# Optimization experiments

Hardware: AMD Instinct MI355X
Metric: run time of the kernel (lower is better)

The kernel has to match this reference:

```python
import jax, jax.numpy as jnp
import numpy as np

DIM = 3072
DIM_HEAD = 128
HEADS = 16
KV_DIM = 2048
INNER = DIM_HEAD * HEADS  # 2048


def layernorm(x, g, b, eps=1e-5):
    mu = jnp.mean(x, axis=-1, keepdims=True)
    var = jnp.mean((x - mu) ** 2, axis=-1, keepdims=True)
    return (x - mu) * jax.lax.rsqrt(var + eps) * g + b


def setup_inputs() -> dict:
    key = jax.random.key(0)
    ks = jax.random.split(key, 6)
    b, n1, n2 = 2, 4096, 1024
    x = jax.random.normal(ks[0], (b, n1, KV_DIM), dtype=jnp.float32)
    latents = jax.random.normal(ks[1], (b, n2, DIM), dtype=jnp.float32)
    # Linear weights stored [in, out] (torch stores [out, in]; math is x @ W)
    Wq = jax.random.normal(ks[2], (DIM, INNER), dtype=jnp.float32) * 0.02
    Wkv = jax.random.normal(ks[3], (KV_DIM, 2 * INNER), dtype=jnp.float32) * 0.02
    Wout = jax.random.normal(ks[4], (INNER, DIM), dtype=jnp.float32) * 0.02
    ln1_g = jnp.ones((KV_DIM,), jnp.float32)
    ln1_b = jnp.zeros((KV_DIM,), jnp.float32)
    ln2_g = jnp.ones((DIM,), jnp.float32)
    ln2_b = jnp.zeros((DIM,), jnp.float32)
    return {"x": x, "latents": latents, "ln1_g": ln1_g, "ln1_b": ln1_b,
            "ln2_g": ln2_g, "ln2_b": ln2_b, "Wq": Wq, "Wkv": Wkv, "Wout": Wout}


def reference(x, latents, ln1_g, ln1_b, ln2_g, ln2_b, Wq, Wkv, Wout):
    b, n2, _ = latents.shape
    xn = layernorm(x, ln1_g, ln1_b)          # (b, n1, kv_dim)
    ln = layernorm(latents, ln2_g, ln2_b)    # (b, n2, dim)
    q = ln @ Wq                               # (b, n2, inner)
    kv = xn @ Wkv                             # (b, n1, 2*inner)
    k, v = jnp.split(kv, 2, axis=-1)
    # (b, seq, h*d) -> (b, h, seq, d)
    def heads(t):
        bs, L, _ = t.shape
        return t.reshape(bs, L, HEADS, DIM_HEAD).transpose(0, 2, 1, 3)
    q, k, v = heads(q), heads(k), heads(v)
    scale = 1.0 / np.sqrt(np.sqrt(DIM_HEAD)).astype(np.float32)
    logits = jnp.einsum('bhqd,bhkd->bhqk', q * scale, k * scale)
    w = jax.nn.softmax(logits.astype(jnp.float32), axis=-1).astype(logits.dtype)
    out = jnp.einsum('bhqk,bhkd->bhqd', w, v)  # (b, h, n2, d)
    out = out.transpose(0, 2, 1, 3).reshape(b, n2, INNER)
    return out @ Wout
```

## Files before the change

### kernel.cpp

```cpp
#include <hip/hip_runtime.h>
#include <stdint.h>

typedef unsigned short u16;
typedef unsigned int u32;
typedef __attribute__((ext_vector_type(4))) float f32x4;
typedef __attribute__((ext_vector_type(8))) __bf16 bf16x8;

#define N1T 4096
#define N2T 1024
#define DIMT 3072
#define KVD 2048
#define INN 2048
#define NH 16
#define DH 128

__device__ __forceinline__ u16 f2bf(float f) {
  u32 u = __builtin_bit_cast(u32, f);
  u = (u + 0x7fffu + ((u >> 16) & 1u)) >> 16;
  return (u16)u;
}

__device__ __forceinline__ u32 cvtpk(float lo, float hi) {
  u32 r;
  asm volatile("v_cvt_pk_bf16_f32 %0, %1, %2" : "=v"(r) : "v"(lo), "v"(hi));
  return r;
}

typedef __attribute__((address_space(1))) void gvoid_t;
typedef __attribute__((address_space(3))) void lvoid_t;

__device__ __forceinline__ void gload16(const void* g, void* l) {
  __builtin_amdgcn_global_load_lds((gvoid_t*)g, (lvoid_t*)l, 16, 0, 0);
}

template<int NV>
__global__ __launch_bounds__(256) void ln_cast_kernel(
    const float* __restrict__ X, const float* __restrict__ G,
    const float* __restrict__ B, u16* __restrict__ out) {
  const int D = NV * 1024;
  const int t = threadIdx.x;
  const size_t row = blockIdx.x;
  const float4* xr = (const float4*)(X + row * D);
  float4 v[NV];
  float s = 0.f, ss = 0.f;
#pragma unroll
  for (int i = 0; i < NV; ++i) {
    v[i] = xr[i * 256 + t];
    s += v[i].x + v[i].y + v[i].z + v[i].w;
    ss += v[i].x * v[i].x + v[i].y * v[i].y + v[i].z * v[i].z + v[i].w * v[i].w;
  }
#pragma unroll
  for (int off = 32; off; off >>= 1) {
    s += __shfl_xor(s, off);
    ss += __shfl_xor(ss, off);
  }
  __shared__ float red[2][4];
  const int wave = t >> 6, lane = t & 63;
  if (lane == 0) { red[0][wave] = s; red[1][wave] = ss; }
  __syncthreads();
  s = red[0][0] + red[0][1] + red[0][2] + red[0][3];
  ss = red[1][0] + red[1][1] + red[1][2] + red[1][3];
  const float mu = s / D;
  const float rstd = rsqrtf(ss / D - mu * mu + 1e-5f);
  u16* orow = out + row * D;
#pragma unroll
  for (int i = 0; i < NV; ++i) {
    const int idx = (i * 256 + t) * 4;
    float4 g4 = *(const float4*)(G + idx);
    float4 b4 = *(const float4*)(B + idx);
    union { ushort4 v4; u16 h[4]; } pk;
    pk.h[0] = f2bf((v[i].x - mu) * rstd * g4.x + b4.x);
    pk.h[1] = f2bf((v[i].y - mu) * rstd * g4.y + b4.y);
    pk.h[2] = f2bf((v[i].z - mu) * rstd * g4.z + b4.z);
    pk.h[3] = f2bf((v[i].w - mu) * rstd * g4.w + b4.w);
    *(ushort4*)(orow + idx) = pk.v4;
  }
}

__global__ __launch_bounds__(256) void tcast_kernel(
    const float* __restrict__ W, u16* __restrict__ WT, int K, int N) {
  __shared__ __align__(16) u16 tile[64][72];
  const int t = threadIdx.x;
  const int k0 = blockIdx.x * 64, n0 = blockIdx.y * 64;
#pragma unroll
  for (int i = 0; i < 4; ++i) {
    int idx = i * 256 + t;
    int r = idx >> 4, c = (idx & 15) << 2;
    float4 v = *(const float4*)(W + (size_t)(k0 + r) * N + n0 + c);
    union { ushort4 v4; u16 h[4]; } pk;
    pk.h[0] = f2bf(v.x); pk.h[1] = f2bf(v.y);
    pk.h[2] = f2bf(v.z); pk.h[3] = f2bf(v.w);
    *(ushort4*)&tile[r][c] = pk.v4;
  }
  __syncthreads();
#pragma unroll
  for (int j = 0; j < 2; ++j) {
    int cid = j * 256 + t;
    int nr = cid >> 3, kc = (cid & 7) << 3;
    union { uint4 v4; u16 h[8]; } pk;
#pragma unroll
    for (int jj = 0; jj < 8; ++jj) pk.h[jj] = tile[kc + jj][nr];
    *(uint4*)(WT + (size_t)(n0 + nr) * K + k0 + kc) = pk.v4;
  }
}

template<int BF16OUT>
__global__ __launch_bounds__(256) void gemm_bt_kernel(
    const u16* __restrict__ A, size_t Az,
    const u16* __restrict__ Bt, size_t Btz,
    void* __restrict__ Cv, size_t Cz,
    int M, int N, int K, float scale) {
  __shared__ __align__(16) u16 As[128 * 64];
  __shared__ __align__(16) u16 Bs[128 * 64];
  A += (size_t)blockIdx.z * Az;
  Bt += (size_t)blockIdx.z * Btz;
  const int t = threadIdx.x, lane = t & 63, wave = t >> 6;
  const int m0 = blockIdx.x * 128, n0 = blockIdx.y * 128;
  const int wr = (wave >> 1) * 64, wc = (wave & 1) * 64;
  const int fr = lane & 15, fk = (lane >> 4) * 8;
  f32x4 acc[4][4];
#pragma unroll
  for (int i = 0; i < 4; ++i)
#pragma unroll
    for (int j = 0; j < 4; ++j)
#pragma unroll
      for (int r = 0; r < 4; ++r) acc[i][j][r] = 0.f;
  const int srow = t >> 3;
  const int scb = (t & 7) * 16;
  const int nk = K >> 6;
  for (int kt = 0; kt < nk; ++kt) {
    const char* Ab = (const char*)(A + (size_t)kt * 64);
    const char* Bb = (const char*)(Bt + (size_t)kt * 64);
#pragma unroll
    for (int r = 0; r < 4; ++r) {
      int row = srow + r * 32;
      gload16(Ab + (size_t)(m0 + row) * K * 2 + scb, (char*)As + t * 16 + r * 4096);
      gload16(Bb + (size_t)(n0 + row) * K * 2 + scb, (char*)Bs + t * 16 + r * 4096);
    }
    __syncthreads();
#pragma unroll
    for (int kk = 0; kk < 2; ++kk) {
      bf16x8 af[4], bfr[4];
#pragma unroll
      for (int i = 0; i < 4; ++i)
        af[i] = *(const bf16x8*)&As[(wr + i * 16 + fr) * 64 + kk * 32 + fk];
#pragma unroll
      for (int j = 0; j < 4; ++j)
        bfr[j] = *(const bf16x8*)&Bs[(wc + j * 16 + fr) * 64 + kk * 32 + fk];
#pragma unroll
      for (int i = 0; i < 4; ++i)
#pragma unroll
        for (int j = 0; j < 4; ++j)
          acc[i][j] = __builtin_amdgcn_mfma_f32_16x16x32_bf16(af[i], bfr[j], acc[i][j], 0, 0, 0);
    }
    __syncthreads();
  }
  const int cr = (lane >> 4) * 4, cc = lane & 15;
#pragma unroll
  for (int i = 0; i < 4; ++i)
#pragma unroll
    for (int j = 0; j < 4; ++j) {
      const int row = m0 + wr + i * 16 + cr;
      const int col = n0 + wc + j * 16 + cc;
      if (BF16OUT) {
        u16* C = (u16*)Cv + (size_t)blockIdx.z * Cz;
#pragma unroll
        for (int r = 0; r < 4; ++r) C[(size_t)(row + r) * N + col] = f2bf(acc[i][j][r] * scale);
      } else {
        float* C = (float*)Cv + (size_t)blockIdx.z * Cz;
#pragma unroll
        for (int r = 0; r < 4; ++r) C[(size_t)(row + r) * N + col] = acc[i][j][r];
      }
    }
}

__device__ __forceinline__ void stage_region(const u16* __restrict__ G, int ldk,
                                             int rowbase, int colbase,
                                             u16* lds, int t) {
  const int srow = t >> 2, sc = t & 3;
  const int swz = (srow >> 1) & 3;
#pragma unroll
  for (int r = 0; r < 2; ++r) {
    int row = r * 128 + srow;
    gload16(G + (size_t)(rowbase + row) * ldk + colbase + (sc ^ swz) * 8,
            (char*)lds + t * 16 + r * 8192);
  }
}

#define GPHASE(MSUB, KK, STAGE_STMT, RELOAD_B, VM0)                               \
  {                                                                               \
    STAGE_STMT;                                                                   \
    const u16* Aarr = (KK) ? A1s : A0s;                                           \
    _Pragma("unroll")                                                             \
    for (int fi = 0; fi < 4; ++fi) {                                              \
      int rowa = RM + (MSUB) * 64 + fi * 16 + fr;                                 \
      af[fi] = *(const bf16x8*)((const char*)Aarr + rowa * 64 +                   \
                                ((q ^ ((rowa >> 1) & 3)) * 16));                  \
    }                                                                             \
    if (RELOAD_B) {                                                               \
      const u16* Barr = (KK) ? B1s : B0s;                                         \
      _Pragma("unroll")                                                           \
      for (int j = 0; j < 4; ++j) {                                               \
        int rowb = RN + j * 16 + fr;                                              \
        bf[j] = *(const bf16x8*)((const char*)Barr + rowb * 64 +                  \
                                 ((q ^ ((rowb >> 1) & 3)) * 16));                 \
      }                                                                           \
    }                                                                             \
    if (VM0) { asm volatile("s_waitcnt vmcnt(0)" ::: "memory"); }                 \
    else     { asm volatile("s_waitcnt vmcnt(2)" ::: "memory"); }                 \
    __builtin_amdgcn_s_barrier();                                                 \
    asm volatile("s_waitcnt lgkmcnt(0)" ::: "memory");                            \
    __builtin_amdgcn_sched_barrier(0);                                            \
    __builtin_amdgcn_s_setprio(1);                                                \
    _Pragma("unroll")                                                             \
    for (int fi = 0; fi < 4; ++fi)                                                \
      _Pragma("unroll")                                                           \
      for (int j = 0; j < 4; ++j)                                                 \
        acc[(MSUB) * 4 + fi][j] = __builtin_amdgcn_mfma_f32_16x16x32_bf16(        \
            af[fi], bf[j], acc[(MSUB) * 4 + fi][j], 0, 0, 0);                     \
    __builtin_amdgcn_s_setprio(0);                                                \
    __builtin_amdgcn_s_barrier();                                                 \
  }

template<int BF16OUT>
__global__ __launch_bounds__(512) void gemm256_kernel(
    const u16* __restrict__ A, size_t Az,
    const u16* __restrict__ Bt, size_t Btz,
    void* __restrict__ Cv, size_t Cz,
    int M, int N, int K, float scale) {
  __shared__ __align__(16) u16 A0s[256 * 32];
  __shared__ __align__(16) u16 A1s[256 * 32];
  __shared__ __align__(16) u16 B0s[256 * 32];
  __shared__ __align__(16) u16 B1s[256 * 32];
  A += (size_t)blockIdx.z * Az;
  Bt += (size_t)blockIdx.z * Btz;
  const int t = threadIdx.x, lane = t & 63, wave = t >> 6;
  const int m0 = blockIdx.x * 256, n0 = blockIdx.y * 256;
  const int RM = (wave >> 2) * 128, RN = (wave & 3) * 64;
  const int fr = lane & 15, q = lane >> 4;
  f32x4 acc[8][4];
#pragma unroll
  for (int i = 0; i < 8; ++i)
#pragma unroll
    for (int j = 0; j < 4; ++j)
#pragma unroll
      for (int r = 0; r < 4; ++r) acc[i][j][r] = 0.f;

  stage_region(Bt, K, n0, 0, B0s, t);
  stage_region(A, K, m0, 0, A0s, t);
  stage_region(Bt, K, n0, 32, B1s, t);
  asm volatile("s_waitcnt vmcnt(0)" ::: "memory");
  __builtin_amdgcn_s_barrier();

  const int nk = K >> 6;
#pragma unroll 1
  for (int kt = 0; kt < nk; ++kt) {
    const bool last = (kt == nk - 1);
    bf16x8 af[4], bf[4];
    GPHASE(0, 0, stage_region(A, K, m0, kt * 64 + 32, A1s, t), true, false)
    GPHASE(1, 0, if (!last) stage_region(Bt, K, n0, (kt + 1) * 64, B0s, t), false, last)
    GPHASE(1, 1, if (!last) stage_region(A, K, m0, (kt + 1) * 64, A0s, t), true, last)
    GPHASE(0, 1, if (!last) stage_region(Bt, K, n0, (kt + 1) * 64 + 32, B1s, t), false, last)
  }

  const int cr = (lane >> 4) * 4, cc = lane & 15;
#pragma unroll
  for (int i = 0; i < 8; ++i)
#pragma unroll
    for (int j = 0; j < 4; ++j) {
      const int row = m0 + RM + i * 16 + cr;
      const int col = n0 + RN + j * 16 + cc;
      if (BF16OUT) {
        u16* C = (u16*)Cv + (size_t)blockIdx.z * Cz;
#pragma unroll
        for (int r = 0; r < 4; ++r) C[(size_t)(row + r) * N + col] = f2bf(acc[i][j][r] * scale);
      } else {
        float* C = (float*)Cv + (size_t)blockIdx.z * Cz;
#pragma unroll
        for (int r = 0; r < 4; ++r) C[(size_t)(row + r) * N + col] = acc[i][j][r];
      }
    }
}

#define KVB 128
__device__ __forceinline__ int swz4(int row) {
  return ((row & 15) ^ (((row >> 4) & 1) << 2)) << 4;
}

__device__ __forceinline__ void stage_kv(const u16* Kbase, const u16* Vbase,
                                         int kv0, char* ks, char* vs, int t) {
  const int col = (t & 15) * 16;
#pragma unroll
  for (int r = 0; r < 4; ++r) {
    int row = (t >> 4) + r * 32;
    gload16((const char*)(Kbase + (size_t)(kv0 + row) * INN) + (col ^ swz4(row)),
            ks + t * 16 + r * 8192);
  }
#pragma unroll
  for (int r = 0; r < 4; ++r) {
    int row = (t >> 4) + r * 32;
    gload16((const char*)(Vbase + (size_t)row * N1T + kv0) + (col ^ swz4(row)),
            vs + t * 16 + r * 8192);
  }
}

__global__ __launch_bounds__(512) void attn_kernel(
    const u16* __restrict__ Q, const u16* __restrict__ Kb,
    const u16* __restrict__ Vt, u16* __restrict__ O) {
  __shared__ __align__(16) u16 Ks[2][KVB * 128];
  __shared__ __align__(16) u16 Vs[2][128 * KVB];
  const int t = threadIdx.x, lane = t & 63, wave = t >> 6;
  const int bid = blockIdx.x;
  const int xcd = bid & 7, idx = bid >> 3;
  const int bh = (xcd << 2) | (idx >> 3);
  const int q0 = (idx & 7) * 128;
  const int b = bh >> 4, h = bh & 15;
  const int fr = lane & 15, quad = lane >> 4;
  const int fk = quad * 8;
  const int frp = fr + (fr & 12);

  bf16x8 qf[4];
  {
    const u16* qrow = Q + (size_t)(b * N2T + q0 + wave * 16 + fr) * INN + h * DH;
#pragma unroll
    for (int c = 0; c < 4; ++c) qf[c] = *(const bf16x8*)(qrow + c * 32 + fk);
  }

  float m_run = -1e30f, l_run = 0.f;
  f32x4 oT[8];
#pragma unroll
  for (int i = 0; i < 8; ++i)
#pragma unroll
    for (int r = 0; r < 4; ++r) oT[i][r] = 0.f;

  const u16* Kbase = Kb + (size_t)(b * N1T) * INN + h * DH;
  const u16* Vbase = Vt + ((size_t)b * INN + h * DH) * N1T;

  const int NT = N1T / KVB;
  int cur = 0;
  stage_kv(Kbase, Vbase, 0, (char*)&Ks[0][0], (char*)&Vs[0][0], t);
  for (int tile = 0; tile < NT; ++tile) {
    if (tile + 1 < NT) {
      stage_kv(Kbase, Vbase, (tile + 1) * KVB, (char*)&Ks[cur ^ 1][0],
               (char*)&Vs[cur ^ 1][0], t);
      asm volatile("s_waitcnt vmcnt(8)" ::: "memory");
    } else {
      asm volatile("s_waitcnt vmcnt(0)" ::: "memory");
    }
    __builtin_amdgcn_s_barrier();
    __builtin_amdgcn_sched_barrier(0);
    const char* KsC = (const char*)&Ks[cur][0];
    const char* VsC = (const char*)&Vs[cur][0];

    f32x4 sT[8];
#pragma unroll
    for (int ni = 0; ni < 8; ++ni) {
#pragma unroll
      for (int r = 0; r < 4; ++r) sT[ni][r] = 0.f;
      const int rowa = (ni >> 1) * 32 + (ni & 1) * 4 + frp;
      const int sz = swz4(rowa);
#pragma unroll
      for (int c = 0; c < 4; ++c) {
        bf16x8 kf = *(const bf16x8*)(KsC + rowa * 256 + ((c * 64 + quad * 16) ^ sz));
        sT[ni] = __builtin_amdgcn_mfma_f32_16x16x32_bf16(kf, qf[c], sT[ni], 0, 0, 0);
      }
    }
    float mt = sT[0][0];
#pragma unroll
    for (int ni = 0; ni < 8; ++ni)
#pragma unroll
      for (int r = 0; r < 4; ++r) mt = fmaxf(mt, sT[ni][r]);
    mt = fmaxf(mt, __shfl_xor(mt, 16));
    mt = fmaxf(mt, __shfl_xor(mt, 32));
    if (!__all(mt <= m_run + 8.f)) {
      float mnew = fmaxf(m_run, mt);
      float alpha = __expf(m_run - mnew);
      m_run = mnew;
      l_run *= alpha;
#pragma unroll
      for (int i = 0; i < 8; ++i)
#pragma unroll
        for (int r = 0; r < 4; ++r) oT[i][r] *= alpha;
    }
    float lt = 0.f;
#pragma unroll
    for (int ni = 0; ni < 8; ++ni)
#pragma unroll
      for (int r = 0; r < 4; ++r) {
        sT[ni][r] = __expf(sT[ni][r] - m_run);
        lt += sT[ni][r];
      }
    lt += __shfl_xor(lt, 16);
    lt += __shfl_xor(lt, 32);
    l_run += lt;
    union { u32 w[4]; bf16x8 v; } pa[4];
#pragma unroll
    for (int kk = 0; kk < 4; ++kk) {
      pa[kk].w[0] = cvtpk(sT[kk * 2][0], sT[kk * 2][1]);
      pa[kk].w[1] = cvtpk(sT[kk * 2][2], sT[kk * 2][3]);
      pa[kk].w[2] = cvtpk(sT[kk * 2 + 1][0], sT[kk * 2 + 1][1]);
      pa[kk].w[3] = cvtpk(sT[kk * 2 + 1][2], sT[kk * 2 + 1][3]);
    }
#pragma unroll
    for (int ni2 = 0; ni2 < 8; ++ni2) {
      const int rowv = ni2 * 16 + fr;
      const int sz = swz4(rowv);
#pragma unroll
      for (int kk = 0; kk < 4; ++kk) {
        bf16x8 vf = *(const bf16x8*)(VsC + rowv * 256 + ((kk * 64 + quad * 16) ^ sz));
        oT[ni2] = __builtin_amdgcn_mfma_f32_16x16x32_bf16(vf, pa[kk].v, oT[ni2], 0, 0, 0);
      }
    }
    __builtin_amdgcn_sched_barrier(0);
    __builtin_amdgcn_s_barrier();
    cur ^= 1;
  }
  const float inv = 1.0f / l_run;
  u16* orow = O + (size_t)(b * N2T + q0 + wave * 16 + fr) * INN + h * DH;
#pragma unroll
  for (int ni2 = 0; ni2 < 8; ++ni2) {
    union { ushort4 v4; u16 hh[4]; } pk;
#pragma unroll
    for (int r = 0; r < 4; ++r) pk.hh[r] = f2bf(oT[ni2][r] * inv);
    *(ushort4*)(orow + ni2 * 16 + quad * 4) = pk.v4;
  }
}

extern "C" void kernel_launch(void* const* d_in, const int* in_sizes, int n_in,
                              void* d_out, int out_size, void* d_ws, size_t ws_size,
                              hipStream_t stream) {
  const float* x = (const float*)d_in[0];
  const float* latents = (const float*)d_in[1];
  const float* ln1g = (const float*)d_in[2];
  const float* ln1b = (const float*)d_in[3];
  const float* ln2g = (const float*)d_in[4];
  const float* ln2b = (const float*)d_in[5];
  const float* Wq = (const float*)d_in[6];
  const float* Wkv = (const float*)d_in[7];
  const float* Wout = (const float*)d_in[8];

  char* w = (char*)d_ws;
  u16* xn = (u16*)w;   w += (size_t)8192 * 2048 * 2;
  u16* lnb = (u16*)w;  w += (size_t)2048 * 3072 * 2;
  u16* WqT = (u16*)w;  w += (size_t)2048 * 3072 * 2;
  u16* WkvT = (u16*)w; w += (size_t)4096 * 2048 * 2;
  u16* WoT = (u16*)w;  w += (size_t)3072 * 2048 * 2;
  u16* qb = (u16*)w;   w += (size_t)2048 * 2048 * 2;
  u16* kb = (u16*)w;   w += (size_t)8192 * 2048 * 2;
  u16* vtb = (u16*)w;  w += (size_t)2 * 2048 * 4096 * 2;
  u16* ab = (u16*)w;   w += (size_t)2048 * 2048 * 2;

  dim3 blk(256);
  tcast_kernel<<<dim3(48, 32), blk, 0, stream>>>(Wq, WqT, 3072, 2048);
  tcast_kernel<<<dim3(32, 64), blk, 0, stream>>>(Wkv, WkvT, 2048, 4096);
  tcast_kernel<<<dim3(32, 48), blk, 0, stream>>>(Wout, WoT, 2048, 3072);
  ln_cast_kernel<2><<<8192, blk, 0, stream>>>(x, ln1g, ln1b, xn);
  ln_cast_kernel<3><<<2048, blk, 0, stream>>>(latents, ln2g, ln2b, lnb);

  const float scale = 0.29730177875068026f;
  gemm_bt_kernel<1><<<dim3(16, 16, 1), blk, 0, stream>>>(
      lnb, 0, WqT, 0, qb, 0, 2048, 2048, 3072, scale);
  gemm256_kernel<1><<<dim3(32, 8, 1), dim3(512), 0, stream>>>(
      xn, 0, WkvT, 0, kb, 0, 8192, 2048, 2048, scale);
  gemm256_kernel<1><<<dim3(8, 16, 2), dim3(512), 0, stream>>>(
      WkvT + (size_t)2048 * 2048, 0, xn, (size_t)4096 * 2048,
      vtb, (size_t)2048 * 4096, 2048, 4096, 2048, 1.0f);
  attn_kernel<<<dim3(256), dim3(512), 0, stream>>>(qb, kb, vtb, ab);
  gemm_bt_kernel<0><<<dim3(16, 24, 1), blk, 0, stream>>>(
      ab, 0, WoT, 0, d_out, 0, 2048, 3072, 2048, 1.0f);
}
```

Before: 402.8 us.

## Split attention KV range in two with 32-row Q per wave and combine kernel

Each attention block now handles 32 query rows per wave over half of the KV sequence, so every K/V tile loaded into LDS is reused for twice as many queries. Partial outputs and running max/sum go to fp32 buffers, and a new combine kernel merges them and writes bf16. The softmax switches to exp2 with log2(e) folded into the Q projection scale, and s_setprio is wrapped around the MFMA phases. The cost is the extra round trip of fp32 partials through memory, one more kernel launch, and higher register pressure from the doubled accumulators. The partial buffers also reuse the start of the workspace, which overlaps xn.

```diff
diff --git a/kernel.cpp b/kernel.cpp
--- a/kernel.cpp
+++ b/kernel.cpp
@@ -18,6 +18,10 @@
   u32 u = __builtin_bit_cast(u32, f);
   u = (u + 0x7fffu + ((u >> 16) & 1u)) >> 16;
   return (u16)u;
+}
+
+__device__ __forceinline__ float exp2_fast(float x) {
+  return __builtin_amdgcn_exp2f(x);
 }
 
 __device__ __forceinline__ u32 cvtpk(float lo, float hi) {
@@ -304,44 +308,54 @@
   }
 }
 
-__global__ __launch_bounds__(512) void attn_kernel(
+__global__ __launch_bounds__(512, 2) void attn_kernel(
     const u16* __restrict__ Q, const u16* __restrict__ Kb,
-    const u16* __restrict__ Vt, u16* __restrict__ O) {
+    const u16* __restrict__ Vt, float* __restrict__ Opart,
+    float* __restrict__ ml) {
   __shared__ __align__(16) u16 Ks[2][KVB * 128];
   __shared__ __align__(16) u16 Vs[2][128 * KVB];
   const int t = threadIdx.x, lane = t & 63, wave = t >> 6;
   const int bid = blockIdx.x;
   const int xcd = bid & 7, idx = bid >> 3;
   const int bh = (xcd << 2) | (idx >> 3);
-  const int q0 = (idx & 7) * 128;
+  const int sub = idx & 7;
+  const int qt = sub >> 1, half = sub & 1;
   const int b = bh >> 4, h = bh & 15;
+  const int q0 = qt * 256 + wave * 32;
   const int fr = lane & 15, quad = lane >> 4;
   const int fk = quad * 8;
   const int frp = fr + (fr & 12);
 
-  bf16x8 qf[4];
+  bf16x8 qf0[4], qf1[4];
   {
-    const u16* qrow = Q + (size_t)(b * N2T + q0 + wave * 16 + fr) * INN + h * DH;
-#pragma unroll
-    for (int c = 0; c < 4; ++c) qf[c] = *(const bf16x8*)(qrow + c * 32 + fk);
-  }
-
-  float m_run = -1e30f, l_run = 0.f;
-  f32x4 oT[8];
-#pragma unroll
-  for (int i = 0; i < 8; ++i)
-#pragma unroll
-    for (int r = 0; r < 4; ++r) oT[i][r] = 0.f;
+    const u16* qr0 = Q + (size_t)(b * N2T + q0 + fr) * INN + h * DH;
+    const u16* qr1 = Q + (size_t)(b * N2T + q0 + 16 + fr) * INN + h * DH;
+#pragma unroll
+    for (int c = 0; c < 4; ++c) {
+      qf0[c] = *(const bf16x8*)(qr0 + c * 32 + fk);
+      qf1[c] = *(const bf16x8*)(qr1 + c * 32 + fk);
+    }
+  }
+
+  float m_run[2] = {-1e30f, -1e30f}, l_run[2] = {0.f, 0.f};
+  f32x4 oT[2][8];
+#pragma unroll
+  for (int f = 0; f < 2; ++f)
+#pragma unroll
+    for (int i = 0; i < 8; ++i)
+#pragma unroll
+      for (int r = 0; r < 4; ++r) oT[f][i][r] = 0.f;
 
   const u16* Kbase = Kb + (size_t)(b * N1T) * INN + h * DH;
   const u16* Vbase = Vt + ((size_t)b * INN + h * DH) * N1T;
-
-  const int NT = N1T / KVB;
+  const int kvb = half * 2048;
+
+  const int NT = 2048 / KVB;
   int cur = 0;
-  stage_kv(Kbase, Vbase, 0, (char*)&Ks[0][0], (char*)&Vs[0][0], t);
+  stage_kv(Kbase, Vbase, kvb, (char*)&Ks[0][0], (char*)&Vs[0][0], t);
   for (int tile = 0; tile < NT; ++tile) {
     if (tile + 1 < NT) {
-      stage_kv(Kbase, Vbase, (tile + 1) * KVB, (char*)&Ks[cur ^ 1][0],
+      stage_kv(Kbase, Vbase, kvb + (tile + 1) * KVB, (char*)&Ks[cur ^ 1][0],
                (char*)&Vs[cur ^ 1][0], t);
       asm volatile("s_waitcnt vmcnt(8)" ::: "memory");
     } else {
@@ -352,55 +366,62 @@
     const char* KsC = (const char*)&Ks[cur][0];
     const char* VsC = (const char*)&Vs[cur][0];
 
-    f32x4 sT[8];
+    f32x4 sT[2][8];
+    __builtin_amdgcn_s_setprio(1);
 #pragma unroll
     for (int ni = 0; ni < 8; ++ni) {
 #pragma unroll
-      for (int r = 0; r < 4; ++r) sT[ni][r] = 0.f;
+      for (int r = 0; r < 4; ++r) { sT[0][ni][r] = 0.f; sT[1][ni][r] = 0.f; }
       const int rowa = (ni >> 1) * 32 + (ni & 1) * 4 + frp;
       const int sz = swz4(rowa);
 #pragma unroll
       for (int c = 0; c < 4; ++c) {
         bf16x8 kf = *(const bf16x8*)(KsC + rowa * 256 + ((c * 64 + quad * 16) ^ sz));
-        sT[ni] = __builtin_amdgcn_mfma_f32_16x16x32_bf16(kf, qf[c], sT[ni], 0, 0, 0);
+        sT[0][ni] = __builtin_amdgcn_mfma_f32_16x16x32_bf16(kf, qf0[c], sT[0][ni], 0, 0, 0);
+        sT[1][ni] = __builtin_amdgcn_mfma_f32_16x16x32_bf16(kf, qf1[c], sT[1][ni], 0, 0, 0);
       }
     }
-    float mt = sT[0][0];
-#pragma unroll
-    for (int ni = 0; ni < 8; ++ni)
-#pragma unroll
-      for (int r = 0; r < 4; ++r) mt = fmaxf(mt, sT[ni][r]);
-    mt = fmaxf(mt, __shfl_xor(mt, 16));
-    mt = fmaxf(mt, __shfl_xor(mt, 32));
-    if (!__all(mt <= m_run + 8.f)) {
-      float mnew = fmaxf(m_run, mt);
-      float alpha = __expf(m_run - mnew);
-      m_run = mnew;
-      l_run *= alpha;
-#pragma unroll
-      for (int i = 0; i < 8; ++i)
-#pragma unroll
-        for (int r = 0; r < 4; ++r) oT[i][r] *= alpha;
-    }
-    float lt = 0.f;
-#pragma unroll
-    for (int ni = 0; ni < 8; ++ni)
-#pragma unroll
-      for (int r = 0; r < 4; ++r) {
-        sT[ni][r] = __expf(sT[ni][r] - m_run);
-        lt += sT[ni][r];
+    __builtin_amdgcn_s_setprio(0);
+    union { u32 w[4]; bf16x8 v; } pa[2][4];
+#pragma unroll
+    for (int f = 0; f < 2; ++f) {
+      float mt = sT[f][0][0];
+#pragma unroll
+      for (int ni = 0; ni < 8; ++ni)
+#pragma unroll
+        for (int r = 0; r < 4; ++r) mt = fmaxf(mt, sT[f][ni][r]);
+      mt = fmaxf(mt, __shfl_xor(mt, 16));
+      mt = fmaxf(mt, __shfl_xor(mt, 32));
+      if (!__all(mt <= m_run[f] + 10.f)) {
+        float mnew = fmaxf(m_run[f], mt);
+        float alpha = exp2_fast(m_run[f] - mnew);
+        m_run[f] = mnew;
+        l_run[f] *= alpha;
+#pragma unroll
+        for (int i = 0; i < 8; ++i)
+#pragma unroll
+          for (int r = 0; r < 4; ++r) oT[f][i][r] *= alpha;
       }
-    lt += __shfl_xor(lt, 16);
-    lt += __shfl_xor(lt, 32);
-    l_run += lt;
-    union { u32 w[4]; bf16x8 v; } pa[4];
-#pragma unroll
-    for (int kk = 0; kk < 4; ++kk) {
-      pa[kk].w[0] = cvtpk(sT[kk * 2][0], sT[kk * 2][1]);
-      pa[kk].w[1] = cvtpk(sT[kk * 2][2], sT[kk * 2][3]);
-      pa[kk].w[2] = cvtpk(sT[kk * 2 + 1][0], sT[kk * 2 + 1][1]);
-      pa[kk].w[3] = cvtpk(sT[kk * 2 + 1][2], sT[kk * 2 + 1][3]);
-    }
+      float lt = 0.f;
+#pragma unroll
+      for (int ni = 0; ni < 8; ++ni)
+#pragma unroll
+        for (int r = 0; r < 4; ++r) {
+          sT[f][ni][r] = exp2_fast(sT[f][ni][r] - m_run[f]);
+          lt += sT[f][ni][r];
+        }
+      lt += __shfl_xor(lt, 16);
+      lt += __shfl_xor(lt, 32);
+      l_run[f] += lt;
+#pragma unroll
+      for (int kk = 0; kk < 4; ++kk) {
+        pa[f][kk].w[0] = cvtpk(sT[f][kk * 2][0], sT[f][kk * 2][1]);
+        pa[f][kk].w[1] = cvtpk(sT[f][kk * 2][2], sT[f][kk * 2][3]);
+        pa[f][kk].w[2] = cvtpk(sT[f][kk * 2 + 1][0], sT[f][kk * 2 + 1][1]);
+        pa[f][kk].w[3] = cvtpk(sT[f][kk * 2 + 1][2], sT[f][kk * 2 + 1][3]);
+      }
+    }
+    __builtin_amdgcn_s_setprio(1);
 #pragma unroll
     for (int ni2 = 0; ni2 < 8; ++ni2) {
       const int rowv = ni2 * 16 + fr;
@@ -408,22 +429,50 @@
 #pragma unroll
       for (int kk = 0; kk < 4; ++kk) {
         bf16x8 vf = *(const bf16x8*)(VsC + rowv * 256 + ((kk * 64 + quad * 16) ^ sz));
-        oT[ni2] = __builtin_amdgcn_mfma_f32_16x16x32_bf16(vf, pa[kk].v, oT[ni2], 0, 0, 0);
+        oT[0][ni2] = __builtin_amdgcn_mfma_f32_16x16x32_bf16(vf, pa[0][kk].v, oT[0][ni2], 0, 0, 0);
+        oT[1][ni2] = __builtin_amdgcn_mfma_f32_16x16x32_bf16(vf, pa[1][kk].v, oT[1][ni2], 0, 0, 0);
       }
     }
+    __builtin_amdgcn_s_setprio(0);
     __builtin_amdgcn_sched_barrier(0);
     __builtin_amdgcn_s_barrier();
     cur ^= 1;
   }
-  const float inv = 1.0f / l_run;
-  u16* orow = O + (size_t)(b * N2T + q0 + wave * 16 + fr) * INN + h * DH;
-#pragma unroll
-  for (int ni2 = 0; ni2 < 8; ++ni2) {
-    union { ushort4 v4; u16 hh[4]; } pk;
-#pragma unroll
-    for (int r = 0; r < 4; ++r) pk.hh[r] = f2bf(oT[ni2][r] * inv);
-    *(ushort4*)(orow + ni2 * 16 + quad * 4) = pk.v4;
-  }
+#pragma unroll
+  for (int f = 0; f < 2; ++f) {
+    const size_t row = (size_t)(b * N2T + q0 + f * 16 + fr) * 16 + h;
+    float* op = Opart + ((size_t)half * 32768 + row) * 128 + quad * 4;
+#pragma unroll
+    for (int ni2 = 0; ni2 < 8; ++ni2) {
+      float4 v4 = {oT[f][ni2][0], oT[f][ni2][1], oT[f][ni2][2], oT[f][ni2][3]};
+      *(float4*)(op + ni2 * 16) = v4;
+    }
+    if (quad == 0) {
+      float2 v2 = {m_run[f], l_run[f]};
+      *(float2*)(ml + ((size_t)half * 32768 + row) * 2) = v2;
+    }
+  }
+}
+
+__global__ __launch_bounds__(256) void combine2_kernel(
+    const float* __restrict__ Opart, const float* __restrict__ ml,
+    u16* __restrict__ ab) {
+  const int tid = blockIdx.x * 256 + threadIdx.x;
+  const int row = tid >> 5;
+  const int c = tid & 31;
+  float2 ml1 = *(const float2*)(ml + (size_t)row * 2);
+  float2 ml2 = *(const float2*)(ml + ((size_t)32768 + row) * 2);
+  float m = fmaxf(ml1.x, ml2.x);
+  float w1 = exp2_fast(ml1.x - m), w2 = exp2_fast(ml2.x - m);
+  float inv = 1.0f / (w1 * ml1.y + w2 * ml2.y);
+  float4 o1 = *(const float4*)(Opart + (size_t)row * 128 + c * 4);
+  float4 o2 = *(const float4*)(Opart + ((size_t)32768 + row) * 128 + c * 4);
+  union { ushort4 v4; u16 hh[4]; } pk;
+  pk.hh[0] = f2bf((w1 * o1.x + w2 * o2.x) * inv);
+  pk.hh[1] = f2bf((w1 * o1.y + w2 * o2.y) * inv);
+  pk.hh[2] = f2bf((w1 * o1.z + w2 * o2.z) * inv);
+  pk.hh[3] = f2bf((w1 * o1.w + w2 * o2.w) * inv);
+  *(ushort4*)(ab + (size_t)(row >> 4) * 2048 + (row & 15) * 128 + c * 4) = pk.v4;
 }
 
 extern "C" void kernel_launch(void* const* d_in, const int* in_sizes, int n_in,
@@ -449,6 +498,8 @@
   u16* kb = (u16*)w;   w += (size_t)8192 * 2048 * 2;
   u16* vtb = (u16*)w;  w += (size_t)2 * 2048 * 4096 * 2;
   u16* ab = (u16*)w;   w += (size_t)2048 * 2048 * 2;
+  float* opart = (float*)d_ws;
+  float* mlbuf = (float*)((char*)d_ws + 33554432);
 
   dim3 blk(256);
   tcast_kernel<<<dim3(48, 32), blk, 0, stream>>>(Wq, WqT, 3072, 2048);
@@ -458,14 +509,16 @@
   ln_cast_kernel<3><<<2048, blk, 0, stream>>>(latents, ln2g, ln2b, lnb);
 
   const float scale = 0.29730177875068026f;
+  const float qscale = scale * 1.4426950408889634f;
   gemm_bt_kernel<1><<<dim3(16, 16, 1), blk, 0, stream>>>(
-      lnb, 0, WqT, 0, qb, 0, 2048, 2048, 3072, scale);
+      lnb, 0, WqT, 0, qb, 0, 2048, 2048, 3072, qscale);
   gemm256_kernel<1><<<dim3(32, 8, 1), dim3(512), 0, stream>>>(
       xn, 0, WkvT, 0, kb, 0, 8192, 2048, 2048, scale);
   gemm256_kernel<1><<<dim3(8, 16, 2), dim3(512), 0, stream>>>(
       WkvT + (size_t)2048 * 2048, 0, xn, (size_t)4096 * 2048,
       vtb, (size_t)2048 * 4096, 2048, 4096, 2048, 1.0f);
-  attn_kernel<<<dim3(256), dim3(512), 0, stream>>>(qb, kb, vtb, ab);
+  attn_kernel<<<dim3(256), dim3(512), 0, stream>>>(qb, kb, vtb, opart, mlbuf);
+  combine2_kernel<<<dim3(4096), blk, 0, stream>>>(opart, mlbuf, ab);
   gemm_bt_kernel<0><<<dim3(16, 24, 1), blk, 0, stream>>>(
       ab, 0, WoT, 0, d_out, 0, 2048, 3072, 2048, 1.0f);
 }
```

Result: no change. 396.7 us (-1.5%).
